# Performance work log

Measured on AMD Instinct MI355X. Metric: run time of the kernel, lower is better.

The kernel has to match this reference:

```python
import jax, jax.numpy as jnp
import numpy as np

B, N, U = 128, 512, 256   # batch, n_facts, units
H1 = 50                    # attention MLP hidden (Dense(50))
STEPS = 3                  # memory_steps hardcoded in __init__


def setup_inputs() -> dict:
    key = jax.random.key(0)
    ks = jax.random.split(key, 8)
    g = lambda k, shp, s: jax.random.normal(k, shp, dtype=jnp.float32) * s
    return {
        "facts": g(ks[0], (B, N, U), 1.0),
        "question": g(ks[1], (B, U), 1.0),
        # attention MLP: Dense(50, tanh) then Dense(1)
        "W1": g(ks[2], (4 * U, H1), 0.02),
        "b1": jnp.zeros((H1,), jnp.float32),
        "W2": g(ks[3], (H1, 1), 0.02),
        "b2": jnp.zeros((1,), jnp.float32),
        # SoftAttnGRU weights (keras GRU layout: [z | r | h] gate blocks)
        "gru_k": g(ks[4], (U, 3 * U), 0.02),
        "gru_rk": g(ks[5], (U, 3 * U), 0.02),
        "gru_b": jnp.zeros((3 * U,), jnp.float32),
        # memory_net: Dense(units, relu) over [memory; episode; question]
        "Wm": g(ks[6], (3 * U, U), 0.02),
        "bm": jnp.zeros((U,), jnp.float32),
    }


def _attn_gru_last(facts, att, gru_k, gru_rk, gru_b):
    """Attention-gated GRU over the fact axis; returns last hidden state.
    h_t = a_t * h~_t + (1 - a_t) * h_{t-1}  (attention replaces the update gate;
    the z-gate block of the keras-layout kernel is present but unused)."""
    Bb, Nn, Uu = facts.shape
    x_proj = jnp.einsum('bnu,uv->bnv', facts, gru_k) + gru_b  # [B,N,3U]
    _, xr, xh = jnp.split(x_proj, 3, axis=-1)
    _, rkr, rkh = jnp.split(gru_rk, 3, axis=1)

    def step(h, xs):
        xr_t, xh_t, a_t = xs                      # [B,U],[B,U],[B,1]
        r = jax.nn.sigmoid(xr_t + h @ rkr)        # reset gate
        hh = jnp.tanh(xh_t + (r * h) @ rkh)       # candidate (reset_after=False)
        h_new = a_t * hh + (1.0 - a_t) * h        # attention-gated update
        return h_new, None

    h0 = jnp.zeros((Bb, Uu), facts.dtype)
    xs = (jnp.swapaxes(xr, 0, 1), jnp.swapaxes(xh, 0, 1), jnp.swapaxes(att, 0, 1))
    h_last, _ = jax.lax.scan(step, h0, xs)
    return h_last


def reference(facts, question, W1, b1, W2, b2, gru_k, gru_rk, gru_b, Wm, bm):
    memory = question
    for _ in range(STEPS):
        q = question[:, None, :]
        m = memory[:, None, :]
        # f_i = [f*q, f*m, |f-q|, |f-m|]  -> [B,N,4U]
        feats = jnp.concatenate(
            [facts * q, facts * m, jnp.abs(facts - q), jnp.abs(facts - m)], axis=-1)
        scores = jnp.tanh(feats @ W1 + b1) @ W2 + b2       # [B,N,1]
        att = jax.nn.softmax(scores[..., 0], axis=1)[..., None]  # softmax over facts
        episode = _attn_gru_last(facts, att, gru_k, gru_rk, gru_b)  # [B,U]
        memory = jax.nn.relu(
            jnp.concatenate([memory, episode, question], axis=1) @ Wm + bm)
    return memory
```

## Files before the change

### kernel.cpp

```cpp
#include <hip/hip_runtime.h>
#include <cstdint>
#include <cstddef>


typedef __bf16 bf16_t;
typedef __attribute__((ext_vector_type(8))) __bf16 bf16x8;
typedef __attribute__((ext_vector_type(4))) __bf16 bf16x4;
typedef __attribute__((ext_vector_type(4))) float f32x4;

static __device__ __forceinline__ f32x4 mfma16(bf16x8 a, bf16x8 b, f32x4 c) {
  return __builtin_amdgcn_mfma_f32_16x16x32_bf16(a, b, c, 0, 0, 0);
}
static __device__ __forceinline__ float fast_rcp(float x) { return __builtin_amdgcn_rcpf(x); }
static __device__ __forceinline__ float sigmoid_f(float x) {
  return fast_rcp(1.f + exp2f(-1.44269504f * x));
}
static __device__ __forceinline__ float tanh_f(float x) {
  float e = exp2f(2.88539008f * x);
  return 1.f - 2.f * fast_rcp(e + 1.f);
}
static __device__ __forceinline__ unsigned short f2bf(float x) {
  __bf16 h = (__bf16)x;
  return __builtin_bit_cast(unsigned short, h);
}
static __device__ __forceinline__ void ldsbar() {
  asm volatile("s_waitcnt lgkmcnt(0)\n\ts_barrier" ::: "memory");
}

static constexpr size_t E_GRUK  = 0;
static constexpr size_t E_RKR   = 131072;
static constexpr size_t E_RKH   = 196608;
static constexpr size_t E_W1F   = 262144;
static constexpr size_t E_WMF   = 327680;
static constexpr size_t E_XR    = 524288;
static constexpr size_t E_XHC   = E_XR  + (size_t)128 * 131072;
static constexpr size_t E_FACTS = E_XHC + (size_t)128 * 131072;
static constexpr size_t E_END   = E_FACTS + (size_t)128 * 131072;
static constexpr size_t F_SCORES = 0;
static constexpr size_t F_MEM    = 65536;

__global__ void prep_weights(const float* __restrict__ gru_k,
                             const float* __restrict__ gru_rk,
                             const float* __restrict__ W1,
                             const float* __restrict__ Wm,
                             bf16_t* __restrict__ ws) {
  size_t idx = (size_t)blockIdx.x * 256 + threadIdx.x;
  if (idx >= 524288) return;
  size_t local; int NT, which;
  if (idx < 131072)      { local = idx;          NT = 32; which = 0; }
  else if (idx < 196608) { local = idx - 131072; NT = 16; which = 1; }
  else if (idx < 262144) { local = idx - 196608; NT = 16; which = 2; }
  else if (idx < 327680) { local = idx - 262144; NT = 4;  which = 3; }
  else                   { local = idx - 327680; NT = 16; which = 4; }
  int j    = (int)(local & 7);
  int lane = (int)((local >> 3) & 63);
  size_t rem = local >> 9;
  int nt = (int)(rem % NT);
  int kt = (int)(rem / NT);
  int k = kt * 32 + (lane >> 4) * 8 + j;
  int n = nt * 16 + (lane & 15);
  float v;
  switch (which) {
    case 0:  v = gru_k[(size_t)k * 768 + 256 + n]; break;
    case 1:  v = gru_rk[(size_t)k * 768 + 256 + n]; break;
    case 2:  v = gru_rk[(size_t)k * 768 + 512 + n]; break;
    case 3:  v = (n < 50) ? W1[(size_t)k * 50 + n] : 0.f; break;
    default: v = Wm[(size_t)k * 256 + n]; break;
  }
  ws[idx] = (__bf16)v;
}

__global__ __launch_bounds__(256)
void xproj_kernel(const float* __restrict__ facts,
                  const float* __restrict__ question,
                  const float* __restrict__ gru_bg,
                  bf16_t* __restrict__ ws,
                  float* __restrict__ mem_ws) {
  const int b = blockIdx.x, s = blockIdx.y;
  const int tid = threadIdx.x, w = tid >> 6, lane = tid & 63;
  const int quad = lane >> 4, col = lane & 15;
  __shared__ float grub[512];
  __shared__ bf16_t fragbuf[4096];
  __shared__ bf16_t xrtrans[4096];
  grub[tid]       = gru_bg[256 + tid];
  grub[256 + tid] = gru_bg[512 + tid];
  if (s == 0) mem_ws[b * 256 + tid] = question[(size_t)b * 256 + tid];
  __syncthreads();

  bf16_t* xr_ws = ws + E_XR   + (size_t)b * 131072;
  bf16_t* xh_ws = ws + E_XHC  + (size_t)b * 131072;
  bf16_t* ff_ws = ws + E_FACTS + (size_t)b * 131072;
  const bf16_t* gbase = ws + E_GRUK;
  const int row = tid >> 4, cseg = tid & 15;

  for (int mt = 0; mt < 4; ++mt) {
    const int Mt = s * 4 + mt;
    const float* src = facts + (((size_t)b * 512) + Mt * 16 + row) * 256 + cseg * 16;
    float v[16];
    #pragma unroll
    for (int i = 0; i < 4; ++i) {
      f32x4 t4 = ((const f32x4*)src)[i];
      v[4 * i] = t4[0]; v[4 * i + 1] = t4[1]; v[4 * i + 2] = t4[2]; v[4 * i + 3] = t4[3];
    }
    #pragma unroll
    for (int half = 0; half < 2; ++half) {
      int u0 = cseg * 16 + half * 8;
      int kt = u0 >> 5, qk = (u0 >> 3) & 3;
      bf16x8 pk;
      #pragma unroll
      for (int j = 0; j < 8; ++j) pk[j] = (__bf16)v[half * 8 + j];
      *(bf16x8*)&fragbuf[((kt * 64) + qk * 16 + row) * 8] = pk;
    }
    ldsbar();
    {
      bf16x8 f0 = *(bf16x8*)&fragbuf[tid * 16];
      bf16x8 f1 = *(bf16x8*)&fragbuf[tid * 16 + 8];
      *(bf16x8*)(ff_ws + (size_t)Mt * 4096 + tid * 16) = f0;
      *(bf16x8*)(ff_ws + (size_t)Mt * 4096 + tid * 16 + 8) = f1;
    }
    bf16x8 af[8];
    #pragma unroll
    for (int kt = 0; kt < 8; ++kt) af[kt] = *(const bf16x8*)&fragbuf[(kt * 64 + lane) * 8];
    f32x4 acc[8];
    #pragma unroll
    for (int nt = 0; nt < 8; ++nt) acc[nt] = (f32x4){0.f, 0.f, 0.f, 0.f};
    #pragma unroll
    for (int kt = 0; kt < 8; ++kt)
      #pragma unroll
      for (int nt = 0; nt < 8; ++nt) {
        bf16x8 g = *(const bf16x8*)(gbase + (((size_t)kt * 32 + (w * 8 + nt)) * 64 + lane) * 8);
        acc[nt] = mfma16(af[kt], g, acc[nt]);
      }
    #pragma unroll
    for (int nt = 0; nt < 8; ++nt) {
      int o = w * 128 + nt * 16 + col;
      float bias = grub[o];
      if (o < 256) {
        int kt = o >> 5, qk = (o >> 3) & 3, j = o & 7;
        #pragma unroll
        for (int r = 0; r < 4; ++r) {
          int tl = quad * 4 + r;
          xrtrans[((kt * 64) + qk * 16 + tl) * 8 + j] = (__bf16)(acc[nt][r] + bias);
        }
      } else {
        int ntx = (o >> 4) - 16;
        unsigned short s0 = f2bf(acc[nt][0] + bias), s1 = f2bf(acc[nt][1] + bias);
        unsigned short s2 = f2bf(acc[nt][2] + bias), s3 = f2bf(acc[nt][3] + bias);
        uint2 pv;
        pv.x = (unsigned)s0 | ((unsigned)s1 << 16);
        pv.y = (unsigned)s2 | ((unsigned)s3 << 16);
        *(uint2*)(xh_ws + ((size_t)Mt * 16 + ntx) * 256 + lane * 4) = pv;
      }
    }
    ldsbar();
    {
      bf16x8 f0 = *(bf16x8*)&xrtrans[tid * 16];
      bf16x8 f1 = *(bf16x8*)&xrtrans[tid * 16 + 8];
      *(bf16x8*)(xr_ws + (size_t)Mt * 4096 + tid * 16) = f0;
      *(bf16x8*)(xr_ws + (size_t)Mt * 4096 + tid * 16 + 8) = f1;
    }
    ldsbar();
  }
}

__global__ __launch_bounds__(256)
void scores_kernel(const float* __restrict__ question,
                   const float* __restrict__ b1g,
                   const float* __restrict__ W2g,
                   const float* __restrict__ b2g,
                   const bf16_t* __restrict__ ws,
                   const float* __restrict__ mem_ws,
                   float* __restrict__ scores_ws) {
  const int b = blockIdx.x, s = blockIdx.y;
  const int tid = threadIdx.x, w = tid >> 6, lane = tid & 63;
  const int quad = lane >> 4, col = lane & 15;
  __shared__ float q_lds[256], mem_lds[256], b1_lds[64], W2_lds[64], score_lds[64];
  __shared__ float b2s;
  q_lds[tid]   = question[(size_t)b * 256 + tid];
  mem_lds[tid] = mem_ws[(size_t)b * 256 + tid];
  if (tid < 64) {
    b1_lds[tid] = (tid < 50) ? b1g[tid] : 0.f;
    W2_lds[tid] = (tid < 50) ? W2g[tid] : 0.f;
  }
  if (tid == 0) b2s = b2g[0];
  __syncthreads();
  if (tid < 64) score_lds[tid] = b2s;
  __syncthreads();

  const bf16_t* ffb = ws + E_FACTS + (size_t)b * 131072 + (size_t)s * 4 * 4096;
  const bf16_t* w1b = ws + E_W1F;

  f32x4 acc[4];
  #pragma unroll
  for (int mt = 0; mt < 4; ++mt) acc[mt] = (f32x4){0.f, 0.f, 0.f, 0.f};

  #pragma unroll 2
  for (int kt = 0; kt < 8; ++kt) {
    bf16x8 wf0 = *(const bf16x8*)(w1b + (((size_t)(kt)      * 4 + w) * 64 + lane) * 8);
    bf16x8 wf1 = *(const bf16x8*)(w1b + (((size_t)(8  + kt) * 4 + w) * 64 + lane) * 8);
    bf16x8 wf2 = *(const bf16x8*)(w1b + (((size_t)(16 + kt) * 4 + w) * 64 + lane) * 8);
    bf16x8 wf3 = *(const bf16x8*)(w1b + (((size_t)(24 + kt) * 4 + w) * 64 + lane) * 8);
    const f32x4* qp = (const f32x4*)&q_lds[kt * 32 + quad * 8];
    const f32x4* mp = (const f32x4*)&mem_lds[kt * 32 + quad * 8];
    f32x4 qa = qp[0], qb = qp[1], ma = mp[0], mb = mp[1];
    float qv[8] = {qa[0],qa[1],qa[2],qa[3],qb[0],qb[1],qb[2],qb[3]};
    float mv[8] = {ma[0],ma[1],ma[2],ma[3],mb[0],mb[1],mb[2],mb[3]};
    #pragma unroll
    for (int mt = 0; mt < 4; ++mt) {
      bf16x8 f8 = *(const bf16x8*)(ffb + (size_t)mt * 4096 + (kt * 64 + lane) * 8);
      bf16x8 a0, a1, a2, a3;
      #pragma unroll
      for (int j = 0; j < 8; ++j) {
        float fu = (float)f8[j];
        a0[j] = (__bf16)(fu * qv[j]);
        a1[j] = (__bf16)(fu * mv[j]);
        a2[j] = (__bf16)fabsf(fu - qv[j]);
        a3[j] = (__bf16)fabsf(fu - mv[j]);
      }
      acc[mt] = mfma16(a0, wf0, acc[mt]);
      acc[mt] = mfma16(a1, wf1, acc[mt]);
      acc[mt] = mfma16(a2, wf2, acc[mt]);
      acc[mt] = mfma16(a3, wf3, acc[mt]);
    }
  }
  int hcol = w * 16 + col;
  float pw2 = W2_lds[hcol], pb1 = b1_lds[hcol];
  #pragma unroll
  for (int mt = 0; mt < 4; ++mt) {
    float p[4];
    #pragma unroll
    for (int r = 0; r < 4; ++r) p[r] = tanh_f(acc[mt][r] + pb1) * pw2;
    #pragma unroll
    for (int r = 0; r < 4; ++r) {
      p[r] += __shfl_xor(p[r], 1, 64);
      p[r] += __shfl_xor(p[r], 2, 64);
      p[r] += __shfl_xor(p[r], 4, 64);
      p[r] += __shfl_xor(p[r], 8, 64);
    }
    if (col == 0) {
      #pragma unroll
      for (int r = 0; r < 4; ++r)
        atomicAdd(&score_lds[mt * 16 + quad * 4 + r], p[r]);
    }
  }
  __syncthreads();
  if (tid < 64) scores_ws[(size_t)b * 512 + s * 64 + tid] = score_lds[tid];
}

__global__ __launch_bounds__(512, 2)
void scan_kernel(const float* __restrict__ question,
                 const float* __restrict__ bmg,
                 const bf16_t* __restrict__ ws,
                 const float* __restrict__ scores_ws,
                 float* __restrict__ mem_ws,
                 float* __restrict__ out,
                 int last) {
  const int b = blockIdx.x;
  const int tid = threadIdx.x, w = tid >> 6, lane = tid & 63;
  const int quad = lane >> 4, col = lane & 15;

  __shared__ bf16_t hb_lds[512];
  __shared__ float aw_lds[512], pt_lds[16];
  __shared__ float q_lds[256], mem_lds[256], bm_lds[256], red[16];
  __shared__ bf16_t fragbuf[8192];

  if (tid < 256) {
    q_lds[tid]   = question[(size_t)b * 256 + tid];
    mem_lds[tid] = mem_ws[(size_t)b * 256 + tid];
    bm_lds[tid]  = bmg[tid];
  }
  hb_lds[tid] = (__bf16)0.f;
  float s0 = scores_ws[(size_t)b * 512 + tid];
  float mx = s0;
  #pragma unroll
  for (int o = 32; o > 0; o >>= 1) mx = fmaxf(mx, __shfl_xor(mx, o, 64));
  if (lane == 0) red[w] = mx;
  __syncthreads();
  float gmax = red[0];
  #pragma unroll
  for (int i = 1; i < 8; ++i) gmax = fmaxf(gmax, red[i]);
  float e0 = __expf(s0 - gmax);
  float sm = e0;
  #pragma unroll
  for (int o = 32; o > 0; o >>= 1) sm += __shfl_xor(sm, o, 64);
  if (lane == 0) red[8 + w] = sm;
  __syncthreads();
  float tot = red[8];
  #pragma unroll
  for (int i = 9; i < 16; ++i) tot += red[i];
  aw_lds[tid] = e0 * fast_rcp(tot);
  ldsbar();
  if (tid < 16) {
    float av[32];
    #pragma unroll
    for (int j = 0; j < 32; ++j) av[j] = aw_lds[tid * 32 + j];
    float suf = 1.f;
    #pragma unroll
    for (int j = 31; j >= 0; --j) {
      aw_lds[tid * 32 + j] = av[j] * suf;
      suf *= (1.f - av[j]);
    }
    pt_lds[tid] = suf;
  }
  ldsbar();

  const bf16_t* xrb = ws + E_XR  + (size_t)b * 131072;
  const bf16_t* xhb = ws + E_XHC + (size_t)b * 131072;
  bf16x8 fr[2][8], fh[2][8];
  {
    const bf16_t* rb = ws + E_RKR;
    const bf16_t* hbw = ws + E_RKH;
    #pragma unroll
    for (int nt = 0; nt < 2; ++nt)
      #pragma unroll
      for (int kt = 0; kt < 8; ++kt) {
        size_t off = (((size_t)kt * 16 + (w * 2 + nt)) * 64 + lane) * 8;
        fr[nt][kt] = *(const bf16x8*)(rb + off);
        fh[nt][kt] = *(const bf16x8*)(hbw + off);
      }
  }
  bf16x8 xf_c[2];
  bf16x4 xh_c[2][2];
  #pragma unroll
  for (int mt = 0; mt < 2; ++mt) {
    xf_c[mt] = *(const bf16x8*)(xrb + (size_t)mt * 4096 + ((size_t)w * 64 + lane) * 8);
    #pragma unroll
    for (int nt = 0; nt < 2; ++nt)
      xh_c[mt][nt] = *(const bf16x4*)(xhb + ((size_t)mt * 16 + w * 2 + nt) * 256 + lane * 4);
  }

  bf16_t* hbc = &hb_lds[0];
  bf16_t* hbn = &hb_lds[256];
  float hs0 = 0.f, hs1 = 0.f;

  for (int ct = 0; ct < 16; ++ct) {
    f32x4 z = (f32x4){0.f,0.f,0.f,0.f};
    f32x4 a0a = z, a0b = z, a1a = z, a1b = z;
    #pragma unroll
    for (int kt = 0; kt < 4; ++kt) {
      bf16x8 hf = *(const bf16x8*)&hbc[kt * 32 + quad * 8];
      a0a = mfma16(hf, fr[0][kt], a0a);
      a1a = mfma16(hf, fr[1][kt], a1a);
    }
    #pragma unroll
    for (int kt = 4; kt < 8; ++kt) {
      bf16x8 hf = *(const bf16x8*)&hbc[kt * 32 + quad * 8];
      a0b = mfma16(hf, fr[0][kt], a0b);
      a1b = mfma16(hf, fr[1][kt], a1b);
    }
    f32x4 ac0 = a0a + a0b, ac1 = a1a + a1b;
    float rv[8];
    #pragma unroll
    for (int j = 0; j < 8; ++j) {
      int c = quad * 8 + j;
      float v0 = __shfl(ac0[0], c & 15, 64);
      float v1 = __shfl(ac1[0], c & 15, 64);
      rv[j] = (c < 16) ? v0 : v1;
    }
    {
      bf16x8 aW = *(const bf16x8*)&hbc[w * 32 + quad * 8];
      #pragma unroll
      for (int mt = 0; mt < 2; ++mt) {
        bf16x8 rh;
        #pragma unroll
        for (int j = 0; j < 8; ++j)
          rh[j] = (__bf16)(sigmoid_f((float)xf_c[mt][j] + rv[j]) * (float)aW[j]);
        *(bf16x8*)&fragbuf[mt * 4096 + (w * 64 + lane) * 8] = rh;
      }
    }
    ldsbar();
    bf16x8 xf_n[2];
    bf16x4 xh_n[2][2];
    {
      int ctn = (ct + 1) & 15;
      #pragma unroll
      for (int mt = 0; mt < 2; ++mt) {
        xf_n[mt] = *(const bf16x8*)(xrb + (size_t)(2 * ctn + mt) * 4096 + ((size_t)w * 64 + lane) * 8);
        #pragma unroll
        for (int nt = 0; nt < 2; ++nt)
          xh_n[mt][nt] = *(const bf16x4*)(xhb + ((size_t)(2 * ctn + mt) * 16 + w * 2 + nt) * 256 + lane * 4);
      }
    }
    f32x4 aH[2][2];
    #pragma unroll
    for (int mt = 0; mt < 2; ++mt) { aH[mt][0] = z; aH[mt][1] = z; }
    #pragma unroll
    for (int mt = 0; mt < 2; ++mt)
      #pragma unroll
      for (int kt = 0; kt < 8; ++kt) {
        bf16x8 a = *(const bf16x8*)&fragbuf[mt * 4096 + (kt * 64 + lane) * 8];
        aH[mt][0] = mfma16(a, fh[0][kt], aH[mt][0]);
        aH[mt][1] = mfma16(a, fh[1][kt], aH[mt][1]);
      }
    const float* awp = &aw_lds[ct * 32];
    f32x4 wq0 = *(const f32x4*)&awp[quad * 4];
    f32x4 wq1 = *(const f32x4*)&awp[16 + quad * 4];
    float Pt = pt_lds[ct];
    float part0 = 0.f, part1 = 0.f;
    #pragma unroll
    for (int r = 0; r < 4; ++r) {
      part0 += wq0[r] * tanh_f((float)xh_c[0][0][r] + aH[0][0][r]);
      part1 += wq0[r] * tanh_f((float)xh_c[0][1][r] + aH[0][1][r]);
      part0 += wq1[r] * tanh_f((float)xh_c[1][0][r] + aH[1][0][r]);
      part1 += wq1[r] * tanh_f((float)xh_c[1][1][r] + aH[1][1][r]);
    }
    part0 += __shfl_xor(part0, 16, 64); part0 += __shfl_xor(part0, 32, 64);
    part1 += __shfl_xor(part1, 16, 64); part1 += __shfl_xor(part1, 32, 64);
    float hn0 = Pt * hs0 + part0;
    float hn1 = Pt * hs1 + part1;
    hs0 = hn0; hs1 = hn1;
    if (quad == 0) {
      hbn[w * 32 + col]      = (__bf16)hn0;
      hbn[w * 32 + 16 + col] = (__bf16)hn1;
    }
    ldsbar();
    { bf16_t* t = hbc; hbc = hbn; hbn = t; }
    #pragma unroll
    for (int mt = 0; mt < 2; ++mt) {
      xf_c[mt] = xf_n[mt];
      xh_c[mt][0] = xh_n[mt][0];
      xh_c[mt][1] = xh_n[mt][1];
    }
  }

  {
    f32x4 am0 = (f32x4){0.f,0.f,0.f,0.f}, am1 = am0;
    const bf16_t* wmb = ws + E_WMF;
    #pragma unroll
    for (int kt = 0; kt < 24; ++kt) {
      bf16x8 a;
      if (kt >= 8 && kt < 16) {
        a = *(const bf16x8*)&hbc[(kt - 8) * 32 + quad * 8];
      } else {
        const float* sv = (kt < 8) ? &mem_lds[kt * 32] : &q_lds[(kt - 16) * 32];
        const f32x4* vp = (const f32x4*)&sv[quad * 8];
        f32x4 va = vp[0], vb = vp[1];
        #pragma unroll
        for (int j = 0; j < 4; ++j) { a[j] = (__bf16)va[j]; a[4 + j] = (__bf16)vb[j]; }
      }
      bf16x8 b0 = *(const bf16x8*)(wmb + (((size_t)kt * 16 + w * 2)     * 64 + lane) * 8);
      bf16x8 b1 = *(const bf16x8*)(wmb + (((size_t)kt * 16 + w * 2 + 1) * 64 + lane) * 8);
      am0 = mfma16(a, b0, am0);
      am1 = mfma16(a, b1, am1);
    }
    if (quad == 0) {
      int v0 = w * 32 + col, v1 = w * 32 + 16 + col;
      float r0 = fmaxf(am0[0] + bm_lds[v0], 0.f);
      float r1 = fmaxf(am1[0] + bm_lds[v1], 0.f);
      mem_ws[(size_t)b * 256 + v0] = r0;
      mem_ws[(size_t)b * 256 + v1] = r1;
      if (last) {
        out[(size_t)b * 256 + v0] = r0;
        out[(size_t)b * 256 + v1] = r1;
      }
    }
  }
}

extern "C" void kernel_launch(void* const* d_in, const int* in_sizes, int n_in,
                              void* d_out, int out_size, void* d_ws, size_t ws_size,
                              hipStream_t stream) {
  (void)in_sizes; (void)n_in; (void)out_size; (void)ws_size;
  const float* facts    = (const float*)d_in[0];
  const float* question = (const float*)d_in[1];
  const float* W1       = (const float*)d_in[2];
  const float* b1       = (const float*)d_in[3];
  const float* W2       = (const float*)d_in[4];
  const float* b2       = (const float*)d_in[5];
  const float* gru_k    = (const float*)d_in[6];
  const float* gru_rk   = (const float*)d_in[7];
  const float* gru_b    = (const float*)d_in[8];
  const float* Wm       = (const float*)d_in[9];
  const float* bm       = (const float*)d_in[10];
  bf16_t* ws = (bf16_t*)d_ws;
  float* fws = (float*)(ws + E_END);
  float* scores_ws = fws + F_SCORES;
  float* mem_ws    = fws + F_MEM;
  float* out = (float*)d_out;

  prep_weights<<<2048, 256, 0, stream>>>(gru_k, gru_rk, W1, Wm, ws);
  xproj_kernel<<<dim3(128, 8), 256, 0, stream>>>(facts, question, gru_b, ws, mem_ws);
  for (int ep = 0; ep < 3; ++ep) {
    scores_kernel<<<dim3(128, 8), 256, 0, stream>>>(question, b1, W2, b2, ws, mem_ws, scores_ws);
    scan_kernel<<<128, 512, 0, stream>>>(question, bm, ws, scores_ws, mem_ws, out, ep == 2);
  }
}
```

Measured before the change: 416.8 us.

## Swizzle LDS staging buffers and prefetch next fact tile in GRU input projection

XOR-swizzles the LDS indices of the fragment and xr transpose buffers to reduce bank conflicts. It prefetches the next 16-row tile of facts into registers while the current tile is processed, which overlaps global load latency with MFMA work. It also drops the trailing barrier and loads A fragments per k-step instead of holding all eight. Removing that barrier relies on the swizzled write/read ordering still being race-free. Holding the prefetch doubles the per-thread fact register footprint.

```diff
diff --git a/kernel.cpp b/kernel.cpp
--- a/kernel.cpp
+++ b/kernel.cpp
@@ -93,54 +93,74 @@
   const bf16_t* gbase = ws + E_GRUK;
   const int row = tid >> 4, cseg = tid & 15;
 
+  int wunit[2];
+  #pragma unroll
+  for (int half = 0; half < 2; ++half) {
+    int u0 = cseg * 16 + half * 8;
+    int kt = u0 >> 5, qk = (u0 >> 3) & 3;
+    int u = kt * 64 + qk * 16 + row;
+    wunit[half] = u ^ kt;
+  }
+
+  float v[16];
+  {
+    const float* src = facts + (((size_t)b * 512) + (s * 4) * 16 + row) * 256 + cseg * 16;
+    #pragma unroll
+    for (int i = 0; i < 4; ++i) {
+      f32x4 t4 = ((const f32x4*)src)[i];
+      v[4*i] = t4[0]; v[4*i+1] = t4[1]; v[4*i+2] = t4[2]; v[4*i+3] = t4[3];
+    }
+  }
+
   for (int mt = 0; mt < 4; ++mt) {
     const int Mt = s * 4 + mt;
-    const float* src = facts + (((size_t)b * 512) + Mt * 16 + row) * 256 + cseg * 16;
-    float v[16];
-    #pragma unroll
-    for (int i = 0; i < 4; ++i) {
-      f32x4 t4 = ((const f32x4*)src)[i];
-      v[4 * i] = t4[0]; v[4 * i + 1] = t4[1]; v[4 * i + 2] = t4[2]; v[4 * i + 3] = t4[3];
-    }
     #pragma unroll
     for (int half = 0; half < 2; ++half) {
-      int u0 = cseg * 16 + half * 8;
-      int kt = u0 >> 5, qk = (u0 >> 3) & 3;
       bf16x8 pk;
       #pragma unroll
       for (int j = 0; j < 8; ++j) pk[j] = (__bf16)v[half * 8 + j];
-      *(bf16x8*)&fragbuf[((kt * 64) + qk * 16 + row) * 8] = pk;
+      *(bf16x8*)&fragbuf[wunit[half] * 8] = pk;
     }
     ldsbar();
+    float vn[16];
+    if (mt < 3) {
+      const float* src = facts + (((size_t)b * 512) + (Mt + 1) * 16 + row) * 256 + cseg * 16;
+      #pragma unroll
+      for (int i = 0; i < 4; ++i) {
+        f32x4 t4 = ((const f32x4*)src)[i];
+        vn[4*i] = t4[0]; vn[4*i+1] = t4[1]; vn[4*i+2] = t4[2]; vn[4*i+3] = t4[3];
+      }
+    }
     {
-      bf16x8 f0 = *(bf16x8*)&fragbuf[tid * 16];
-      bf16x8 f1 = *(bf16x8*)&fragbuf[tid * 16 + 8];
-      *(bf16x8*)(ff_ws + (size_t)Mt * 4096 + tid * 16) = f0;
-      *(bf16x8*)(ff_ws + (size_t)Mt * 4096 + tid * 16 + 8) = f1;
-    }
-    bf16x8 af[8];
-    #pragma unroll
-    for (int kt = 0; kt < 8; ++kt) af[kt] = *(const bf16x8*)&fragbuf[(kt * 64 + lane) * 8];
+      int p0 = 2 * tid, p1 = 2 * tid + 1;
+      bf16x8 f0 = *(bf16x8*)&fragbuf[(p0 ^ (p0 >> 6)) * 8];
+      bf16x8 f1 = *(bf16x8*)&fragbuf[(p1 ^ (p1 >> 6)) * 8];
+      *(bf16x8*)(ff_ws + (size_t)Mt * 4096 + (size_t)p0 * 8) = f0;
+      *(bf16x8*)(ff_ws + (size_t)Mt * 4096 + (size_t)p1 * 8) = f1;
+    }
     f32x4 acc[8];
     #pragma unroll
     for (int nt = 0; nt < 8; ++nt) acc[nt] = (f32x4){0.f, 0.f, 0.f, 0.f};
     #pragma unroll
-    for (int kt = 0; kt < 8; ++kt)
+    for (int kt = 0; kt < 8; ++kt) {
+      bf16x8 af = *(const bf16x8*)&fragbuf[(size_t)(((kt * 64 + lane) ^ kt)) * 8];
       #pragma unroll
       for (int nt = 0; nt < 8; ++nt) {
         bf16x8 g = *(const bf16x8*)(gbase + (((size_t)kt * 32 + (w * 8 + nt)) * 64 + lane) * 8);
-        acc[nt] = mfma16(af[kt], g, acc[nt]);
-      }
+        acc[nt] = mfma16(af, g, acc[nt]);
+      }
+    }
     #pragma unroll
     for (int nt = 0; nt < 8; ++nt) {
       int o = w * 128 + nt * 16 + col;
       float bias = grub[o];
       if (o < 256) {
-        int kt = o >> 5, qk = (o >> 3) & 3, j = o & 7;
+        int ktA = o >> 5, qkA = (o >> 3) & 3, j = o & 7;
         #pragma unroll
         for (int r = 0; r < 4; ++r) {
-          int tl = quad * 4 + r;
-          xrtrans[((kt * 64) + qk * 16 + tl) * 8 + j] = (__bf16)(acc[nt][r] + bias);
+          int u = ktA * 64 + qkA * 16 + (quad * 4 + r);
+          int us = u ^ ((u >> 4) & 3);
+          xrtrans[us * 8 + j] = (__bf16)(acc[nt][r] + bias);
         }
       } else {
         int ntx = (o >> 4) - 16;
@@ -154,12 +174,16 @@
     }
     ldsbar();
     {
-      bf16x8 f0 = *(bf16x8*)&xrtrans[tid * 16];
-      bf16x8 f1 = *(bf16x8*)&xrtrans[tid * 16 + 8];
-      *(bf16x8*)(xr_ws + (size_t)Mt * 4096 + tid * 16) = f0;
-      *(bf16x8*)(xr_ws + (size_t)Mt * 4096 + tid * 16 + 8) = f1;
-    }
-    ldsbar();
+      int p0 = 2 * tid, p1 = 2 * tid + 1;
+      bf16x8 f0 = *(bf16x8*)&xrtrans[(p0 ^ ((p0 >> 4) & 3)) * 8];
+      bf16x8 f1 = *(bf16x8*)&xrtrans[(p1 ^ ((p1 >> 4) & 3)) * 8];
+      *(bf16x8*)(xr_ws + (size_t)Mt * 4096 + (size_t)p0 * 8) = f0;
+      *(bf16x8*)(xr_ws + (size_t)Mt * 4096 + (size_t)p1 * 8) = f1;
+    }
+    if (mt < 3) {
+      #pragma unroll
+      for (int i = 0; i < 16; ++i) v[i] = vn[i];
+    }
   }
 }
 
```

After: 474.3 us. 13.8% more time.
